# Performance work log

Measured on AMD Instinct MI355X. Metric: run time of the kernel, lower is better.

## Reference

```python
import jax, jax.numpy as jnp
import numpy as np

C = 512
GROUPS = 4
EPS = 1e-6


def group_norm(x, w, b):
    # x: [B, C, L]
    B, Ch, L = x.shape
    xg = x.reshape(B, GROUPS, Ch // GROUPS, L)
    mean = xg.mean(axis=(2, 3), keepdims=True)
    var = xg.var(axis=(2, 3), keepdims=True)
    xn = ((xg - mean) * jax.lax.rsqrt(var + EPS)).reshape(B, Ch, L)
    return xn * w[None, :, None] + b[None, :, None]


def conv1x1(x, w, b):
    # 1x1 Conv1d == channel mixing: w [Cout, Cin], x [B, Cin, L]
    return jnp.einsum('oc,bcl->bol', w, x) + b[None, :, None]


def setup_inputs() -> dict:
    key = jax.random.key(0)
    ks = jax.random.split(key, 11)
    s = 1.0 / np.sqrt(C)
    return {
        'x': jax.random.normal(ks[0], (8, C, 2048), dtype=jnp.float32),
        'gn_w': jnp.ones((C,), jnp.float32),
        'gn_b': jnp.zeros((C,), jnp.float32),
        'qw': jax.random.uniform(ks[1], (C, C), jnp.float32, -s, s),
        'qb': jax.random.uniform(ks[2], (C,), jnp.float32, -s, s),
        'kw': jax.random.uniform(ks[3], (C, C), jnp.float32, -s, s),
        'kb': jax.random.uniform(ks[4], (C,), jnp.float32, -s, s),
        'vw': jax.random.uniform(ks[5], (C, C), jnp.float32, -s, s),
        'vb': jax.random.uniform(ks[6], (C,), jnp.float32, -s, s),
        'pw': jax.random.uniform(ks[7], (C, C), jnp.float32, -s, s),
        'pb': jax.random.uniform(ks[8], (C,), jnp.float32, -s, s),
    }


def reference(x, gn_w, gn_b, qw, qb, kw, kb, vw, vb, pw, pb):
    scale = x.shape[1] ** (-0.5)
    xn = group_norm(x, gn_w, gn_b)
    q = conv1x1(xn, qw, qb)
    k = conv1x1(xn, kw, kb)
    v = conv1x1(xn, vw, vb)
    attn = jnp.einsum('bci,bcj->bij', q, k) * scale  # [B, L, L]
    attn = jax.nn.softmax(attn, axis=2)
    out = jnp.einsum('bij,bcj->bci', attn, v)
    out = conv1x1(out, pw, pb)
    return x + out
```

## Files before the change

### kernel.cpp

```cpp
#include <hip/hip_runtime.h>

#define BB 8
#define CC 512
#define LL 2048
#define GG 4
#define CPG 128

typedef _Float16 f16;
typedef _Float16 f16x4 __attribute__((ext_vector_type(4)));
typedef _Float16 f16x8 __attribute__((ext_vector_type(8)));
typedef float f32x4 __attribute__((ext_vector_type(4)));

__device__ __forceinline__ void gload_lds16(const f16* g, f16* l)
{
    __builtin_amdgcn_global_load_lds(
        (__attribute__((address_space(1))) void*)g,
        (__attribute__((address_space(3))) void*)l, 16, 0, 0);
}

__global__ __launch_bounds__(256) void convert_gn(
    const float* __restrict__ qw, const float* __restrict__ kw,
    const float* __restrict__ vw, const float* __restrict__ pw,
    const float* __restrict__ qb, const float* __restrict__ kb,
    const float* __restrict__ x,
    f16* __restrict__ Wqk, f16* __restrict__ Wv, f16* __restrict__ Wp,
    float* __restrict__ qkb, float2* __restrict__ part)
{
    int bid = blockIdx.x;
    if (bid < 256) {
        int j = bid * 256 + threadIdx.x;
        int i = j * 4;
        float4 q4 = *(const float4*)(qw + i);
        float4 k4 = *(const float4*)(kw + i);
        float4 v4 = *(const float4*)(vw + i);
        float4 p4 = *(const float4*)(pw + i);
        f16x4 o;
        o[0] = (f16)q4.x; o[1] = (f16)q4.y; o[2] = (f16)q4.z; o[3] = (f16)q4.w;
        *(f16x4*)(Wqk + i) = o;
        o[0] = (f16)k4.x; o[1] = (f16)k4.y; o[2] = (f16)k4.z; o[3] = (f16)k4.w;
        *(f16x4*)(Wqk + CC * CC + i) = o;
        o[0] = (f16)v4.x; o[1] = (f16)v4.y; o[2] = (f16)v4.z; o[3] = (f16)v4.w;
        *(f16x4*)(Wv + i) = o;
        o[0] = (f16)p4.x; o[1] = (f16)p4.y; o[2] = (f16)p4.z; o[3] = (f16)p4.w;
        *(f16x4*)(Wp + i) = o;
        if (j < CC) { qkb[j] = qb[j]; qkb[CC + j] = kb[j]; }
    } else {
        int r = bid - 256;
        int s = r & 31, g = (r >> 5) & 3, b = r >> 7;
        const float4* p = (const float4*)(x + (size_t)b * CC * LL
                                            + (size_t)g * CPG * LL + (size_t)s * 8192);
        float sum = 0.f, sq = 0.f;
        for (int i = threadIdx.x; i < 2048; i += 256) {
            float4 v = p[i];
            sum += v.x + v.y + v.z + v.w;
            sq  += v.x * v.x + v.y * v.y + v.z * v.z + v.w * v.w;
        }
        for (int o = 32; o; o >>= 1) { sum += __shfl_xor(sum, o); sq += __shfl_xor(sq, o); }
        __shared__ float2 red[4];
        int wave = threadIdx.x >> 6, lane = threadIdx.x & 63;
        if (lane == 0) red[wave] = make_float2(sum, sq);
        __syncthreads();
        if (threadIdx.x == 0) {
            float S = red[0].x + red[1].x + red[2].x + red[3].x;
            float Q = red[0].y + red[1].y + red[2].y + red[3].y;
            part[((size_t)b * GG + g) * 32 + s] = make_float2(S, Q);
        }
    }
}

__global__ __launch_bounds__(256) void gn_norm_t(
    const float* __restrict__ x, const float2* __restrict__ part,
    const float* __restrict__ gw, const float* __restrict__ gb,
    f16* __restrict__ xnT)
{
    __shared__ float t[64][65];
    __shared__ float2 stLds;
    int l0 = blockIdx.x * 64, c0 = blockIdx.y * 64, b = blockIdx.z;
    int tid = threadIdx.x;
    if (tid < 32) {
        float2 p = part[((size_t)b * GG + (c0 >> 7)) * 32 + tid];
        float s = p.x, q = p.y;
        for (int o = 16; o; o >>= 1) { s += __shfl_xor(s, o); q += __shfl_xor(q, o); }
        if (tid == 0) {
            const float invN = 1.0f / (float)(CPG * LL);
            float mean = s * invN;
            float var  = q * invN - mean * mean;
            stLds = make_float2(mean, rsqrtf(var + 1e-6f));
        }
    }
    __syncthreads();
    float2 st = stLds;
    const float* xb = x + (size_t)b * CC * LL;
    {
        int c = tid >> 2, lb = (tid & 3) * 16;
        float g = gw[c0 + c], b2 = gb[c0 + c];
        const float4* src = (const float4*)(xb + (size_t)(c0 + c) * LL + l0 + lb);
#pragma unroll
        for (int q = 0; q < 4; ++q) {
            float4 v = src[q];
            int l = lb + q * 4;
            t[c][l + 0] = (v.x - st.x) * st.y * g + b2;
            t[c][l + 1] = (v.y - st.x) * st.y * g + b2;
            t[c][l + 2] = (v.z - st.x) * st.y * g + b2;
            t[c][l + 3] = (v.w - st.x) * st.y * g + b2;
        }
    }
    __syncthreads();
    f16* o = xnT + (size_t)b * LL * CC;
    {
        int c8 = (tid & 7) * 8;
#pragma unroll
        for (int h = 0; h < 2; ++h) {
            int l = (tid >> 3) + h * 32;
            f16x8 v;
#pragma unroll
            for (int u = 0; u < 8; ++u) v[u] = (f16)t[c8 + u][l];
            *(f16x8*)(o + (size_t)(l0 + l) * CC + c0 + c8) = v;
        }
    }
}

template<int NBT, int BIAS_MODE, bool RESID, bool SOFTEXP, bool ROWSCALE, typename OUT_T>
__global__ __launch_bounds__(256, 2) void gemm_bt(
    const f16* __restrict__ A, size_t sA,
    const f16* __restrict__ B, size_t sB,
    OUT_T* __restrict__ Co, size_t sC,
    const float* __restrict__ resid, size_t sR,
    const float* __restrict__ bias,
    float* __restrict__ rowpart,
    int M, int N, int K, int lda, int ldb, int ldc, float alpha)
{
    constexpr int BN = NBT * 32;

    const int tid  = threadIdx.x;
    const int lane = tid & 63;
    const int wave = tid >> 6;
    const int wr = wave >> 1, wc = wave & 1;
    const int l15 = lane & 15, lhi = lane >> 4;

    const int GX = gridDim.x, GXY = gridDim.x * gridDim.y;
    const int nwg = GXY * gridDim.z;
    int lin = blockIdx.z * GXY + blockIdx.y * GX + blockIdx.x;
    int logical = (lin & 7) * (nwg >> 3) + (lin >> 3);
    const int bz = logical / GXY;
    int rem = logical - bz * GXY;
    const int bm = rem / GX;
    const int bn = rem - bm * GX;

    A  += (size_t)bz * sA;
    B  += (size_t)bz * sB;
    Co += (size_t)bz * sC;

    __shared__ f16 ldsA[128 * 64];
    __shared__ f16 ldsB[BN * 64];
    __shared__ float rsl[128];

    f32x4 acc[4][NBT] = {};

    if constexpr (ROWSCALE) {
        if (tid < 128) {
            const float* rp = rowpart + ((size_t)bz * M + bm * 128 + tid) * 8;
            float s = 0.f;
#pragma unroll
            for (int k = 0; k < 8; ++k) s += rp[k];
            rsl[tid] = 1.0f / s;
        }
    }

    const int srcColE = ((lane & 7) ^ (lane >> 3)) * 8;
    const int rowBase = wave * 8 + (lane >> 3);
    const f16* Ag = A + (size_t)(bm * 128 + rowBase) * lda + srcColE;
    const f16* Bg = B + (size_t)(bn * BN  + rowBase) * ldb + srcColE;

    for (int k0 = 0; k0 < K; k0 += 64) {
#pragma unroll
        for (int it = 0; it < 4; ++it)
            gload_lds16(Ag + (size_t)(it * 32) * lda + k0,
                        (f16*)((char*)ldsA + it * 4096 + wave * 1024));
#pragma unroll
        for (int it = 0; it < NBT; ++it)
            gload_lds16(Bg + (size_t)(it * 32) * ldb + k0,
                        (f16*)((char*)ldsB + it * 4096 + wave * 1024));
        __syncthreads();
#pragma unroll
        for (int kk = 0; kk < 64; kk += 32) {
            const int kb2 = (kk + lhi * 8) * 2;
            f16x8 af[4], bfr[NBT];
#pragma unroll
            for (int m = 0; m < 4; ++m) {
                int row = wr * 64 + m * 16 + l15;
                int phys = ((row * 128 + kb2) ^ ((row & 7) << 4)) >> 1;
                af[m] = *(const f16x8*)(ldsA + phys);
            }
#pragma unroll
            for (int n = 0; n < NBT; ++n) {
                int row = wc * (NBT * 16) + n * 16 + l15;
                int phys = ((row * 128 + kb2) ^ ((row & 7) << 4)) >> 1;
                bfr[n] = *(const f16x8*)(ldsB + phys);
            }
#pragma unroll
            for (int m = 0; m < 4; ++m)
#pragma unroll
                for (int n = 0; n < NBT; ++n)
                    acc[m][n] = __builtin_amdgcn_mfma_f32_16x16x32_f16(
                        af[m], bfr[n], acc[m][n], 0, 0, 0);
        }
        __syncthreads();
    }

    if constexpr (SOFTEXP) {
        __shared__ float rs2[2][128];
        float rowacc[16];
#pragma unroll
        for (int i = 0; i < 16; ++i) rowacc[i] = 0.f;
#pragma unroll
        for (int m = 0; m < 4; ++m) {
#pragma unroll
            for (int n = 0; n < NBT; ++n) {
                int col = bn * BN + wc * (NBT * 16) + n * 16 + l15;
#pragma unroll
                for (int r = 0; r < 4; ++r) {
                    int row = bm * 128 + wr * 64 + m * 16 + lhi * 4 + r;
                    float e = __expf(fminf(acc[m][n][r] * alpha, 11.0f));
                    rowacc[m * 4 + r] += e;
                    Co[(size_t)row * ldc + col] = (OUT_T)e;
                }
            }
        }
#pragma unroll
        for (int off = 1; off < 16; off <<= 1)
#pragma unroll
            for (int i = 0; i < 16; ++i)
                rowacc[i] += __shfl_xor(rowacc[i], off);
        if (l15 == 0) {
#pragma unroll
            for (int i = 0; i < 16; ++i)
                rs2[wc][wr * 64 + (i >> 2) * 16 + lhi * 4 + (i & 3)] = rowacc[i];
        }
        __syncthreads();
        if (tid < 128) {
            int row = bm * 128 + tid;
            rowpart[((size_t)bz * M + row) * gridDim.x + bn] =
                rs2[0][tid] + rs2[1][tid];
        }
    } else {
#pragma unroll
        for (int m = 0; m < 4; ++m) {
#pragma unroll
            for (int n = 0; n < NBT; ++n) {
                int col = bn * BN + wc * (NBT * 16) + n * 16 + l15;
#pragma unroll
                for (int r = 0; r < 4; ++r) {
                    int row = bm * 128 + wr * 64 + m * 16 + lhi * 4 + r;
                    float v = acc[m][n][r] * alpha;
                    if (BIAS_MODE == 1) v += bias[row];
                    if (BIAS_MODE == 2) v += bias[col];
                    if (ROWSCALE) v *= rsl[row - bm * 128];
                    if (RESID) v += resid[(size_t)bz * sR + (size_t)row * ldc + col];
                    Co[(size_t)row * ldc + col] = (OUT_T)v;
                }
            }
        }
    }
}

__global__ void fill_marker(float* out, int n)
{
    int i = blockIdx.x * 256 + threadIdx.x;
    if (i < n) out[i] = 12345.0f;
}

extern "C" void kernel_launch(void* const* d_in, const int* in_sizes, int n_in,
                              void* d_out, int out_size, void* d_ws, size_t ws_size,
                              hipStream_t stream)
{
    const float* x  = (const float*)d_in[0];
    const float* gw = (const float*)d_in[1];
    const float* gb = (const float*)d_in[2];
    const float* qw = (const float*)d_in[3];
    const float* qb = (const float*)d_in[4];
    const float* kw = (const float*)d_in[5];
    const float* kb = (const float*)d_in[6];
    const float* vw = (const float*)d_in[7];
    const float* vb = (const float*)d_in[8];
    const float* pw = (const float*)d_in[9];
    const float* pb = (const float*)d_in[10];
    float* out = (float*)d_out;

    char* w = (char*)d_ws;
    float2* part  = (float2*)w;
    f16* Wqk  = (f16*)(w + 16384);
    f16* Wv   = Wqk + (size_t)1024 * CC;
    f16* Wp   = Wv  + (size_t)CC * CC;
    float* qkb = (float*)(Wp + (size_t)CC * CC);
    f16* xnT  = (f16*)((char*)qkb + 4096);
    f16* QK   = xnT + (size_t)BB * LL * CC;
    f16* Vm   = QK  + (size_t)BB * LL * 1024;
    f16* Pm   = Vm  + (size_t)BB * CC * LL;
    float* rowpart = (float*)(Pm + (size_t)BB * LL * LL);
    f16* O2   = xnT;
    size_t need = (size_t)((char*)(rowpart + (size_t)BB * LL * 8) - w);
    if (ws_size < need) {
        fill_marker<<<(out_size + 255) / 256, 256, 0, stream>>>(out, out_size);
        return;
    }

    convert_gn<<<dim3(1280), 256, 0, stream>>>(
        qw, kw, vw, pw, qb, kb, x, Wqk, Wv, Wp, qkb, part);
    gn_norm_t<<<dim3(LL / 64, CC / 64, BB), 256, 0, stream>>>(x, part, gw, gb, xnT);

    gemm_bt<8, 2, false, false, false, f16><<<dim3(1024 / 256, LL / 128, BB), 256, 0, stream>>>(
        xnT, (size_t)LL * CC, Wqk, 0, QK, (size_t)LL * 1024, nullptr, 0, qkb,
        nullptr,
        LL, 1024, CC, CC, CC, 1024, 1.0f);

    gemm_bt<4, 1, false, false, false, f16><<<dim3(LL / 128, CC / 128, BB), 256, 0, stream>>>(
        Wv, 0, xnT, (size_t)LL * CC, Vm, (size_t)CC * LL, nullptr, 0, vb,
        nullptr,
        CC, LL, CC, CC, CC, LL, 1.0f);

    gemm_bt<8, 0, false, true, false, f16><<<dim3(LL / 256, LL / 128, BB), 256, 0, stream>>>(
        QK, (size_t)LL * 1024, QK + CC, (size_t)LL * 1024, Pm, (size_t)LL * LL,
        nullptr, 0, nullptr,
        rowpart,
        LL, LL, CC, 1024, 1024, LL, 0.04419417382415922f);

    gemm_bt<4, 0, false, false, true, f16><<<dim3(CC / 128, LL / 128, BB), 256, 0, stream>>>(
        Pm, (size_t)LL * LL, Vm, (size_t)CC * LL, O2, (size_t)LL * CC,
        nullptr, 0, nullptr,
        rowpart,
        LL, CC, LL, LL, LL, CC, 1.0f);

    gemm_bt<4, 1, true, false, false, float><<<dim3(LL / 128, CC / 128, BB), 256, 0, stream>>>(
        Wp, 0, O2, (size_t)LL * CC, out, (size_t)CC * LL, x, (size_t)CC * LL, pb,
        nullptr,
        CC, LL, CC, CC, CC, LL, 1.0f);
}
```

Measured before the change: 153.0 us.

## Add double-buffered 512-thread pipelined GEMM for QK, attention and PV stages

```diff
diff --git a/kernel.cpp b/kernel.cpp
--- a/kernel.cpp
+++ b/kernel.cpp
@@ -120,23 +120,17 @@
     }
 }
 
-template<int NBT, int BIAS_MODE, bool RESID, bool SOFTEXP, bool ROWSCALE, typename OUT_T>
-__global__ __launch_bounds__(256, 2) void gemm_bt(
+template<int BIAS_MODE, bool SOFTEXP, bool ROWSCALE, typename OUT_T>
+__global__ __launch_bounds__(512, 2) void gemm_pipe(
     const f16* __restrict__ A, size_t sA,
     const f16* __restrict__ B, size_t sB,
     OUT_T* __restrict__ Co, size_t sC,
-    const float* __restrict__ resid, size_t sR,
-    const float* __restrict__ bias,
-    float* __restrict__ rowpart,
-    int M, int N, int K, int lda, int ldb, int ldc, float alpha)
-{
-    constexpr int BN = NBT * 32;
-
-    const int tid  = threadIdx.x;
-    const int lane = tid & 63;
-    const int wave = tid >> 6;
-    const int wr = wave >> 1, wc = wave & 1;
+    const float* __restrict__ bias, float* __restrict__ rowpart,
+    int M, int K, int lda, int ldb, int ldc, float alpha)
+{
+    const int tid = threadIdx.x, lane = tid & 63, w = tid >> 6;
     const int l15 = lane & 15, lhi = lane >> 4;
+    const int wr = w >> 2, wc = w & 3;
 
     const int GX = gridDim.x, GXY = gridDim.x * gridDim.y;
     const int nwg = GXY * gridDim.z;
@@ -147,15 +141,16 @@
     const int bm = rem / GX;
     const int bn = rem - bm * GX;
 
-    A  += (size_t)bz * sA;
-    B  += (size_t)bz * sB;
+    A  += (size_t)bz * sA + (size_t)(bm * 128) * lda;
+    B  += (size_t)bz * sB + (size_t)(bn * 256) * ldb;
     Co += (size_t)bz * sC;
 
-    __shared__ f16 ldsA[128 * 64];
-    __shared__ f16 ldsB[BN * 64];
+    __shared__ f16 ldsA[2][128 * 64];
+    __shared__ f16 ldsB[2][256 * 64];
+    __shared__ float rs[4][128];
     __shared__ float rsl[128];
 
-    f32x4 acc[4][NBT] = {};
+    f32x4 acc[4][4] = {};
 
     if constexpr (ROWSCALE) {
         if (tid < 128) {
@@ -168,56 +163,126 @@
     }
 
     const int srcColE = ((lane & 7) ^ (lane >> 3)) * 8;
-    const int rowBase = wave * 8 + (lane >> 3);
-    const f16* Ag = A + (size_t)(bm * 128 + rowBase) * lda + srcColE;
-    const f16* Bg = B + (size_t)(bn * BN  + rowBase) * ldb + srcColE;
-
-    for (int k0 = 0; k0 < K; k0 += 64) {
-#pragma unroll
-        for (int it = 0; it < 4; ++it)
-            gload_lds16(Ag + (size_t)(it * 32) * lda + k0,
-                        (f16*)((char*)ldsA + it * 4096 + wave * 1024));
-#pragma unroll
-        for (int it = 0; it < NBT; ++it)
-            gload_lds16(Bg + (size_t)(it * 32) * ldb + k0,
-                        (f16*)((char*)ldsB + it * 4096 + wave * 1024));
-        __syncthreads();
-#pragma unroll
-        for (int kk = 0; kk < 64; kk += 32) {
-            const int kb2 = (kk + lhi * 8) * 2;
-            f16x8 af[4], bfr[NBT];
-#pragma unroll
-            for (int m = 0; m < 4; ++m) {
-                int row = wr * 64 + m * 16 + l15;
-                int phys = ((row * 128 + kb2) ^ ((row & 7) << 4)) >> 1;
-                af[m] = *(const f16x8*)(ldsA + phys);
-            }
-#pragma unroll
-            for (int n = 0; n < NBT; ++n) {
-                int row = wc * (NBT * 16) + n * 16 + l15;
-                int phys = ((row * 128 + kb2) ^ ((row & 7) << 4)) >> 1;
-                bfr[n] = *(const f16x8*)(ldsB + phys);
-            }
-#pragma unroll
-            for (int m = 0; m < 4; ++m)
-#pragma unroll
-                for (int n = 0; n < NBT; ++n)
+    const int sub = (w & 3) * 8 + (lane >> 3);
+    const int half = w >> 2;
+    const int ldst = half * 8192 + (w & 3) * 1024;
+
+    auto S_A1 = [&](int t) {
+        gload_lds16(A + (size_t)(half * 64 + sub) * lda + t * 64 + srcColE,
+                    (f16*)((char*)ldsA[t & 1] + ldst)); };
+    auto S_B1 = [&](int t) {
+        gload_lds16(B + (size_t)(half * 64 + sub) * ldb + t * 64 + srcColE,
+                    (f16*)((char*)ldsB[t & 1] + ldst)); };
+    auto S_B2 = [&](int t) {
+        gload_lds16(B + (size_t)(128 + half * 64 + sub) * ldb + t * 64 + srcColE,
+                    (f16*)((char*)ldsB[t & 1] + 16384 + ldst)); };
+    auto S_B1b = [&](int t) {
+        gload_lds16(B + (size_t)(half * 64 + 32 + sub) * ldb + t * 64 + srcColE,
+                    (f16*)((char*)ldsB[t & 1] + 4096 + ldst)); };
+    auto S_B2b = [&](int t) {
+        gload_lds16(B + (size_t)(128 + half * 64 + 32 + sub) * ldb + t * 64 + srcColE,
+                    (f16*)((char*)ldsB[t & 1] + 20480 + ldst)); };
+    auto S_A1b = [&](int t) {
+        gload_lds16(A + (size_t)(half * 64 + 32 + sub) * lda + t * 64 + srcColE,
+                    (f16*)((char*)ldsA[t & 1] + 4096 + ldst)); };
+
+    auto rd = [&](const f16* tile, int row, int byteCol) -> f16x8 {
+        return *(const f16x8*)((const char*)tile
+            + (((row << 7) + byteCol) ^ ((row & 7) << 4)));
+    };
+
+    const int NT = K >> 6;
+
+    S_A1(0); S_B1(0); S_B2(0); S_B1b(0); S_B2b(0); S_A1b(0);
+    asm volatile("s_waitcnt vmcnt(3)" ::: "memory");
+    __builtin_amdgcn_s_barrier();
+
+    for (int t = 0; t < NT; ++t) {
+        const f16* cA = ldsA[t & 1];
+        const f16* cB = ldsB[t & 1];
+        const bool st = (t < NT - 1);
+        f16x8 a01[2][2], a23[2][2], b01[2][2], b23[2][2];
+#pragma unroll
+        for (int m = 0; m < 2; ++m)
+#pragma unroll
+            for (int kk = 0; kk < 2; ++kk)
+                a01[m][kk] = rd(cA, wr * 64 + m * 16 + l15, kk * 64 + lhi * 16);
+#pragma unroll
+        for (int n = 0; n < 2; ++n)
+#pragma unroll
+            for (int kk = 0; kk < 2; ++kk)
+                b01[n][kk] = rd(cB, wc * 64 + n * 16 + l15, kk * 64 + lhi * 16);
+        if (st) { S_A1(t + 1); S_B1(t + 1); S_B2(t + 1); }
+        asm volatile("s_waitcnt lgkmcnt(0)" ::: "memory");
+        __builtin_amdgcn_sched_barrier(0);
+        __builtin_amdgcn_s_setprio(1);
+#pragma unroll
+        for (int m = 0; m < 2; ++m)
+#pragma unroll
+            for (int n = 0; n < 2; ++n)
+#pragma unroll
+                for (int kk = 0; kk < 2; ++kk)
                     acc[m][n] = __builtin_amdgcn_mfma_f32_16x16x32_f16(
-                        af[m], bfr[n], acc[m][n], 0, 0, 0);
-        }
-        __syncthreads();
+                        a01[m][kk], b01[n][kk], acc[m][n], 0, 0, 0);
+        __builtin_amdgcn_s_setprio(0);
+        if (st) asm volatile("s_waitcnt vmcnt(4)" ::: "memory");
+        else    asm volatile("s_waitcnt vmcnt(1)" ::: "memory");
+        __builtin_amdgcn_s_barrier();
+#pragma unroll
+        for (int n = 0; n < 2; ++n)
+#pragma unroll
+            for (int kk = 0; kk < 2; ++kk)
+                b23[n][kk] = rd(cB, wc * 64 + 32 + n * 16 + l15, kk * 64 + lhi * 16);
+        if (st) { S_B1b(t + 1); S_B2b(t + 1); }
+        asm volatile("s_waitcnt lgkmcnt(0)" ::: "memory");
+        __builtin_amdgcn_sched_barrier(0);
+        __builtin_amdgcn_s_setprio(1);
+#pragma unroll
+        for (int m = 0; m < 2; ++m)
+#pragma unroll
+            for (int n = 0; n < 2; ++n)
+#pragma unroll
+                for (int kk = 0; kk < 2; ++kk)
+                    acc[m][n + 2] = __builtin_amdgcn_mfma_f32_16x16x32_f16(
+                        a01[m][kk], b23[n][kk], acc[m][n + 2], 0, 0, 0);
+        __builtin_amdgcn_s_setprio(0);
+        if (st) asm volatile("s_waitcnt vmcnt(5)" ::: "memory");
+        else    asm volatile("s_waitcnt vmcnt(0)" ::: "memory");
+        __builtin_amdgcn_s_barrier();
+#pragma unroll
+        for (int m = 0; m < 2; ++m)
+#pragma unroll
+            for (int kk = 0; kk < 2; ++kk)
+                a23[m][kk] = rd(cA, wr * 64 + 32 + m * 16 + l15, kk * 64 + lhi * 16);
+        if (st) { S_A1b(t + 1); }
+        asm volatile("s_waitcnt lgkmcnt(0)" ::: "memory");
+        __builtin_amdgcn_sched_barrier(0);
+        __builtin_amdgcn_s_setprio(1);
+#pragma unroll
+        for (int m = 0; m < 2; ++m)
+#pragma unroll
+            for (int n = 0; n < 2; ++n)
+#pragma unroll
+                for (int kk = 0; kk < 2; ++kk) {
+                    acc[m + 2][n] = __builtin_amdgcn_mfma_f32_16x16x32_f16(
+                        a23[m][kk], b01[n][kk], acc[m + 2][n], 0, 0, 0);
+                    acc[m + 2][n + 2] = __builtin_amdgcn_mfma_f32_16x16x32_f16(
+                        a23[m][kk], b23[n][kk], acc[m + 2][n + 2], 0, 0, 0);
+                }
+        __builtin_amdgcn_s_setprio(0);
+        if (st) asm volatile("s_waitcnt vmcnt(3)" ::: "memory");
+        __builtin_amdgcn_s_barrier();
     }
 
     if constexpr (SOFTEXP) {
-        __shared__ float rs2[2][128];
         float rowacc[16];
 #pragma unroll
         for (int i = 0; i < 16; ++i) rowacc[i] = 0.f;
 #pragma unroll
         for (int m = 0; m < 4; ++m) {
 #pragma unroll
-            for (int n = 0; n < NBT; ++n) {
-                int col = bn * BN + wc * (NBT * 16) + n * 16 + l15;
+            for (int n = 0; n < 4; ++n) {
+                int col = bn * 256 + wc * 64 + n * 16 + l15;
 #pragma unroll
                 for (int r = 0; r < 4; ++r) {
                     int row = bm * 128 + wr * 64 + m * 16 + lhi * 4 + r;
@@ -235,30 +300,119 @@
         if (l15 == 0) {
 #pragma unroll
             for (int i = 0; i < 16; ++i)
-                rs2[wc][wr * 64 + (i >> 2) * 16 + lhi * 4 + (i & 3)] = rowacc[i];
+                rs[wc][wr * 64 + (i >> 2) * 16 + lhi * 4 + (i & 3)] = rowacc[i];
         }
         __syncthreads();
         if (tid < 128) {
             int row = bm * 128 + tid;
             rowpart[((size_t)bz * M + row) * gridDim.x + bn] =
-                rs2[0][tid] + rs2[1][tid];
+                rs[0][tid] + rs[1][tid] + rs[2][tid] + rs[3][tid];
         }
     } else {
 #pragma unroll
         for (int m = 0; m < 4; ++m) {
 #pragma unroll
-            for (int n = 0; n < NBT; ++n) {
-                int col = bn * BN + wc * (NBT * 16) + n * 16 + l15;
+            for (int n = 0; n < 4; ++n) {
+                int col = bn * 256 + wc * 64 + n * 16 + l15;
 #pragma unroll
                 for (int r = 0; r < 4; ++r) {
                     int row = bm * 128 + wr * 64 + m * 16 + lhi * 4 + r;
                     float v = acc[m][n][r] * alpha;
-                    if (BIAS_MODE == 1) v += bias[row];
                     if (BIAS_MODE == 2) v += bias[col];
                     if (ROWSCALE) v *= rsl[row - bm * 128];
-                    if (RESID) v += resid[(size_t)bz * sR + (size_t)row * ldc + col];
                     Co[(size_t)row * ldc + col] = (OUT_T)v;
                 }
+            }
+        }
+    }
+}
+
+template<int BIAS_MODE, bool RESID, typename OUT_T>
+__global__ __launch_bounds__(256, 2) void gemm_bt(
+    const f16* __restrict__ A, size_t sA,
+    const f16* __restrict__ B, size_t sB,
+    OUT_T* __restrict__ Co, size_t sC,
+    const float* __restrict__ resid, size_t sR,
+    const float* __restrict__ bias,
+    int M, int N, int K, int lda, int ldb, int ldc, float alpha)
+{
+    const int tid  = threadIdx.x;
+    const int lane = tid & 63;
+    const int wave = tid >> 6;
+    const int wr = wave >> 1, wc = wave & 1;
+    const int l15 = lane & 15, lhi = lane >> 4;
+
+    const int GX = gridDim.x, GXY = gridDim.x * gridDim.y;
+    const int nwg = GXY * gridDim.z;
+    int lin = blockIdx.z * GXY + blockIdx.y * GX + blockIdx.x;
+    int logical = (lin & 7) * (nwg >> 3) + (lin >> 3);
+    const int bz = logical / GXY;
+    int rem = logical - bz * GXY;
+    const int bm = rem / GX;
+    const int bn = rem - bm * GX;
+
+    A  += (size_t)bz * sA;
+    B  += (size_t)bz * sB;
+    Co += (size_t)bz * sC;
+
+    __shared__ f16 ldsA[128 * 64];
+    __shared__ f16 ldsB[128 * 64];
+
+    f32x4 acc[4][4] = {};
+
+    const int srcColE = ((lane & 7) ^ (lane >> 3)) * 8;
+    const int rowBase = wave * 8 + (lane >> 3);
+    const f16* Ag = A + (size_t)(bm * 128 + rowBase) * lda + srcColE;
+    const f16* Bg = B + (size_t)(bn * 128 + rowBase) * ldb + srcColE;
+
+    for (int k0 = 0; k0 < K; k0 += 64) {
+#pragma unroll
+        for (int it = 0; it < 4; ++it) {
+            gload_lds16(Ag + (size_t)(it * 32) * lda + k0,
+                        (f16*)((char*)ldsA + it * 4096 + wave * 1024));
+            gload_lds16(Bg + (size_t)(it * 32) * ldb + k0,
+                        (f16*)((char*)ldsB + it * 4096 + wave * 1024));
+        }
+        __syncthreads();
+#pragma unroll
+        for (int kk = 0; kk < 64; kk += 32) {
+            const int kb2 = (kk + lhi * 8) * 2;
+            f16x8 af[4], bfr[4];
+#pragma unroll
+            for (int m = 0; m < 4; ++m) {
+                int row = wr * 64 + m * 16 + l15;
+                int phys = ((row * 128 + kb2) ^ ((row & 7) << 4)) >> 1;
+                af[m] = *(const f16x8*)(ldsA + phys);
+            }
+#pragma unroll
+            for (int n = 0; n < 4; ++n) {
+                int row = wc * 64 + n * 16 + l15;
+                int phys = ((row * 128 + kb2) ^ ((row & 7) << 4)) >> 1;
+                bfr[n] = *(const f16x8*)(ldsB + phys);
+            }
+#pragma unroll
+            for (int m = 0; m < 4; ++m)
+#pragma unroll
+                for (int n = 0; n < 4; ++n)
+                    acc[m][n] = __builtin_amdgcn_mfma_f32_16x16x32_f16(
+                        af[m], bfr[n], acc[m][n], 0, 0, 0);
+        }
+        __syncthreads();
+    }
+
+#pragma unroll
+    for (int m = 0; m < 4; ++m) {
+#pragma unroll
+        for (int n = 0; n < 4; ++n) {
+            int col = bn * 128 + wc * 64 + n * 16 + l15;
+#pragma unroll
+            for (int r = 0; r < 4; ++r) {
+                int row = bm * 128 + wr * 64 + m * 16 + lhi * 4 + r;
+                float v = acc[m][n][r] * alpha;
+                if (BIAS_MODE == 1) v += bias[row];
+                if (BIAS_MODE == 2) v += bias[col];
+                if (RESID) v += resid[(size_t)bz * sR + (size_t)row * ldc + col];
+                Co[(size_t)row * ldc + col] = (OUT_T)v;
             }
         }
     }
@@ -309,30 +463,25 @@
         qw, kw, vw, pw, qb, kb, x, Wqk, Wv, Wp, qkb, part);
     gn_norm_t<<<dim3(LL / 64, CC / 64, BB), 256, 0, stream>>>(x, part, gw, gb, xnT);
 
-    gemm_bt<8, 2, false, false, false, f16><<<dim3(1024 / 256, LL / 128, BB), 256, 0, stream>>>(
-        xnT, (size_t)LL * CC, Wqk, 0, QK, (size_t)LL * 1024, nullptr, 0, qkb,
-        nullptr,
-        LL, 1024, CC, CC, CC, 1024, 1.0f);
-
-    gemm_bt<4, 1, false, false, false, f16><<<dim3(LL / 128, CC / 128, BB), 256, 0, stream>>>(
+    gemm_pipe<2, false, false, f16><<<dim3(1024 / 256, LL / 128, BB), 512, 0, stream>>>(
+        xnT, (size_t)LL * CC, Wqk, 0, QK, (size_t)LL * 1024, qkb, nullptr,
+        LL, CC, CC, CC, 1024, 1.0f);
+
+    gemm_bt<1, false, f16><<<dim3(LL / 128, CC / 128, BB), 256, 0, stream>>>(
         Wv, 0, xnT, (size_t)LL * CC, Vm, (size_t)CC * LL, nullptr, 0, vb,
-        nullptr,
         CC, LL, CC, CC, CC, LL, 1.0f);
 
-    gemm_bt<8, 0, false, true, false, f16><<<dim3(LL / 256, LL / 128, BB), 256, 0, stream>>>(
+    gemm_pipe<0, true, false, f16><<<dim3(LL / 256, LL / 128, BB), 512, 0, stream>>>(
         QK, (size_t)LL * 1024, QK + CC, (size_t)LL * 1024, Pm, (size_t)LL * LL,
-        nullptr, 0, nullptr,
-        rowpart,
-        LL, LL, CC, 1024, 1024, LL, 0.04419417382415922f);
-
-    gemm_bt<4, 0, false, false, true, f16><<<dim3(CC / 128, LL / 128, BB), 256, 0, stream>>>(
+        nullptr, rowpart,
+        LL, CC, 1024, 1024, LL, 0.04419417382415922f);
+
+    gemm_pipe<0, false, true, f16><<<dim3(CC / 256, LL / 128, BB), 512, 0, stream>>>(
         Pm, (size_t)LL * LL, Vm, (size_t)CC * LL, O2, (size_t)LL * CC,
-        nullptr, 0, nullptr,
-        rowpart,
-        LL, CC, LL, LL, LL, CC, 1.0f);
-
-    gemm_bt<4, 1, true, false, false, float><<<dim3(LL / 128, CC / 128, BB), 256, 0, stream>>>(
+        nullptr, rowpart,
+        LL, LL, LL, LL, CC, 1.0f);
+
+    gemm_bt<1, true, float><<<dim3(LL / 128, CC / 128, BB), 256, 0, stream>>>(
         Wp, 0, O2, (size_t)LL * CC, out, (size_t)CC * LL, x, (size_t)CC * LL, pb,
-        nullptr,
         CC, LL, CC, CC, CC, LL, 1.0f);
 }
```

Result: slower. 180.9 us (+18.3%).

## Fold Q and K projections into a precomputed Wq^T·Wk matrix for attention

Applied to the files above, without the earlier changes.

```diff
diff --git a/kernel.cpp b/kernel.cpp
--- a/kernel.cpp
+++ b/kernel.cpp
@@ -21,46 +21,72 @@
 __global__ __launch_bounds__(256) void convert_gn(
     const float* __restrict__ qw, const float* __restrict__ kw,
     const float* __restrict__ vw, const float* __restrict__ pw,
-    const float* __restrict__ qb, const float* __restrict__ kb,
+    const float* __restrict__ qb,
     const float* __restrict__ x,
-    f16* __restrict__ Wqk, f16* __restrict__ Wv, f16* __restrict__ Wp,
-    float* __restrict__ qkb, float2* __restrict__ part)
+    f16* __restrict__ WqT, f16* __restrict__ WkT,
+    f16* __restrict__ Wv, f16* __restrict__ Wp,
+    float* __restrict__ c1, float2* __restrict__ part)
 {
     int bid = blockIdx.x;
+    int tid = threadIdx.x;
     if (bid < 256) {
-        int j = bid * 256 + threadIdx.x;
-        int i = j * 4;
-        float4 q4 = *(const float4*)(qw + i);
-        float4 k4 = *(const float4*)(kw + i);
+        int i = (bid * 256 + tid) * 4;
         float4 v4 = *(const float4*)(vw + i);
         float4 p4 = *(const float4*)(pw + i);
         f16x4 o;
-        o[0] = (f16)q4.x; o[1] = (f16)q4.y; o[2] = (f16)q4.z; o[3] = (f16)q4.w;
-        *(f16x4*)(Wqk + i) = o;
-        o[0] = (f16)k4.x; o[1] = (f16)k4.y; o[2] = (f16)k4.z; o[3] = (f16)k4.w;
-        *(f16x4*)(Wqk + CC * CC + i) = o;
         o[0] = (f16)v4.x; o[1] = (f16)v4.y; o[2] = (f16)v4.z; o[3] = (f16)v4.w;
         *(f16x4*)(Wv + i) = o;
         o[0] = (f16)p4.x; o[1] = (f16)p4.y; o[2] = (f16)p4.z; o[3] = (f16)p4.w;
         *(f16x4*)(Wp + i) = o;
-        if (j < CC) { qkb[j] = qb[j]; qkb[CC + j] = kb[j]; }
+    } else if (bid < 384) {
+        const float* src = (bid < 320) ? qw : kw;
+        f16* dst = (bid < 320) ? WqT : WkT;
+        int t = (bid - 256) & 63;
+        int o0 = (t & 7) * 64, a0 = (t >> 3) * 64;
+        __shared__ float ts[64][65];
+        {
+            int r = tid >> 2, c4 = (tid & 3) * 16;
+#pragma unroll
+            for (int e4 = 0; e4 < 4; ++e4) {
+                float4 v = *(const float4*)(src + (size_t)(o0 + r) * CC + a0 + c4 + e4 * 4);
+                ts[r][c4 + e4 * 4 + 0] = v.x; ts[r][c4 + e4 * 4 + 1] = v.y;
+                ts[r][c4 + e4 * 4 + 2] = v.z; ts[r][c4 + e4 * 4 + 3] = v.w;
+            }
+        }
+        __syncthreads();
+        {
+            int j8 = (tid & 7) * 8;
+#pragma unroll
+            for (int h = 0; h < 2; ++h) {
+                int ai = (tid >> 3) + h * 32;
+                f16x8 v;
+#pragma unroll
+                for (int e = 0; e < 8; ++e) v[e] = (f16)ts[j8 + e][ai];
+                *(f16x8*)(dst + (size_t)(a0 + ai) * CC + o0 + j8) = v;
+            }
+        }
+    } else if (bid < 386) {
+        int b = (bid - 384) * 256 + tid;
+        float s = 0.f;
+        for (int o = 0; o < CC; ++o) s += kw[(size_t)o * CC + b] * qb[o];
+        c1[b] = s;
     } else {
-        int r = bid - 256;
+        int r = bid - 386;
         int s = r & 31, g = (r >> 5) & 3, b = r >> 7;
         const float4* p = (const float4*)(x + (size_t)b * CC * LL
                                             + (size_t)g * CPG * LL + (size_t)s * 8192);
         float sum = 0.f, sq = 0.f;
-        for (int i = threadIdx.x; i < 2048; i += 256) {
+        for (int i = tid; i < 2048; i += 256) {
             float4 v = p[i];
             sum += v.x + v.y + v.z + v.w;
             sq  += v.x * v.x + v.y * v.y + v.z * v.z + v.w * v.w;
         }
         for (int o = 32; o; o >>= 1) { sum += __shfl_xor(sum, o); sq += __shfl_xor(sq, o); }
         __shared__ float2 red[4];
-        int wave = threadIdx.x >> 6, lane = threadIdx.x & 63;
+        int wave = tid >> 6, lane = tid & 63;
         if (lane == 0) red[wave] = make_float2(sum, sq);
         __syncthreads();
-        if (threadIdx.x == 0) {
+        if (tid == 0) {
             float S = red[0].x + red[1].x + red[2].x + red[3].x;
             float Q = red[0].y + red[1].y + red[2].y + red[3].y;
             part[((size_t)b * GG + g) * 32 + s] = make_float2(S, Q);
@@ -120,7 +146,8 @@
     }
 }
 
-template<int NBT, int BIAS_MODE, bool RESID, bool SOFTEXP, bool ROWSCALE, typename OUT_T>
+template<int NBT, int BIAS_MODE, bool RESID, bool SOFTEXP, bool ROWSCALE,
+         bool ROWDOT, typename OUT_T>
 __global__ __launch_bounds__(256, 2) void gemm_bt(
     const f16* __restrict__ A, size_t sA,
     const f16* __restrict__ B, size_t sB,
@@ -128,6 +155,8 @@
     const float* __restrict__ resid, size_t sR,
     const float* __restrict__ bias,
     float* __restrict__ rowpart,
+    const float* __restrict__ c1d, float* __restrict__ colb_out,
+    const float* __restrict__ colb_in,
     int M, int N, int K, int lda, int ldb, int ldc, float alpha)
 {
     constexpr int BN = NBT * 32;
@@ -154,8 +183,11 @@
     __shared__ f16 ldsA[128 * 64];
     __shared__ f16 ldsB[BN * 64];
     __shared__ float rsl[128];
+    __shared__ float c1L[ROWDOT ? 512 : 1];
+    __shared__ float cbL[SOFTEXP ? 256 : 1];
 
     f32x4 acc[4][NBT] = {};
+    float rdot[4] = {0.f, 0.f, 0.f, 0.f};
 
     if constexpr (ROWSCALE) {
         if (tid < 128) {
@@ -166,6 +198,13 @@
             rsl[tid] = 1.0f / s;
         }
     }
+    if constexpr (ROWDOT) {
+        c1L[tid] = c1d[tid];
+        c1L[tid + 256] = c1d[tid + 256];
+    }
+    if constexpr (SOFTEXP) {
+        cbL[tid] = alpha * colb_in[(size_t)bz * N + bn * BN + tid];
+    }
 
     const int srcColE = ((lane & 7) ^ (lane >> 3)) * 8;
     const int rowBase = wave * 8 + (lane >> 3);
@@ -198,6 +237,14 @@
                 int phys = ((row * 128 + kb2) ^ ((row & 7) << 4)) >> 1;
                 bfr[n] = *(const f16x8*)(ldsB + phys);
             }
+            if constexpr (ROWDOT) {
+                int kbase = k0 + kk + lhi * 8;
+#pragma unroll
+                for (int m = 0; m < 4; ++m)
+#pragma unroll
+                    for (int e = 0; e < 8; ++e)
+                        rdot[m] += c1L[kbase + e] * (float)af[m][e];
+            }
 #pragma unroll
             for (int m = 0; m < 4; ++m)
 #pragma unroll
@@ -208,6 +255,19 @@
         __syncthreads();
     }
 
+    if constexpr (ROWDOT) {
+#pragma unroll
+        for (int m = 0; m < 4; ++m) {
+            rdot[m] += __shfl_xor(rdot[m], 16);
+            rdot[m] += __shfl_xor(rdot[m], 32);
+        }
+        if (wc == 0 && lhi == 0 && bn == 0) {
+#pragma unroll
+            for (int m = 0; m < 4; ++m)
+                colb_out[(size_t)bz * M + bm * 128 + wr * 64 + m * 16 + l15] = rdot[m];
+        }
+    }
+
     if constexpr (SOFTEXP) {
         __shared__ float rs2[2][128];
         float rowacc[16];
@@ -217,11 +277,12 @@
         for (int m = 0; m < 4; ++m) {
 #pragma unroll
             for (int n = 0; n < NBT; ++n) {
-                int col = bn * BN + wc * (NBT * 16) + n * 16 + l15;
+                int colL = wc * (NBT * 16) + n * 16 + l15;
+                int col = bn * BN + colL;
 #pragma unroll
                 for (int r = 0; r < 4; ++r) {
                     int row = bm * 128 + wr * 64 + m * 16 + lhi * 4 + r;
-                    float e = __expf(fminf(acc[m][n][r] * alpha, 11.0f));
+                    float e = __expf(fminf(acc[m][n][r] * alpha + cbL[colL], 11.0f));
                     rowacc[m * 4 + r] += e;
                     Co[(size_t)row * ldc + col] = (OUT_T)e;
                 }
@@ -280,7 +341,7 @@
     const float* qw = (const float*)d_in[3];
     const float* qb = (const float*)d_in[4];
     const float* kw = (const float*)d_in[5];
-    const float* kb = (const float*)d_in[6];
+    const float* kb = (const float*)d_in[6];  (void)kb;
     const float* vw = (const float*)d_in[7];
     const float* vb = (const float*)d_in[8];
     const float* pw = (const float*)d_in[9];
@@ -288,51 +349,60 @@
     float* out = (float*)d_out;
 
     char* w = (char*)d_ws;
-    float2* part  = (float2*)w;
-    f16* Wqk  = (f16*)(w + 16384);
-    f16* Wv   = Wqk + (size_t)1024 * CC;
+    float2* part = (float2*)w;
+    f16* WqT  = (f16*)(w + 16384);
+    f16* WkT  = WqT + (size_t)CC * CC;
+    f16* Wv   = WkT + (size_t)CC * CC;
     f16* Wp   = Wv  + (size_t)CC * CC;
-    float* qkb = (float*)(Wp + (size_t)CC * CC);
-    f16* xnT  = (f16*)((char*)qkb + 4096);
-    f16* QK   = xnT + (size_t)BB * LL * CC;
-    f16* Vm   = QK  + (size_t)BB * LL * 1024;
+    f16* Mf   = Wp  + (size_t)CC * CC;
+    float* c1 = (float*)(Mf + (size_t)CC * CC);
+    f16* xnT  = (f16*)((char*)c1 + 4096);
+    f16* ktT  = xnT + (size_t)BB * LL * CC;
+    f16* Vm   = ktT + (size_t)BB * LL * CC;
     f16* Pm   = Vm  + (size_t)BB * CC * LL;
     float* rowpart = (float*)(Pm + (size_t)BB * LL * LL);
+    float* colb    = rowpart + (size_t)BB * LL * 8;
     f16* O2   = xnT;
-    size_t need = (size_t)((char*)(rowpart + (size_t)BB * LL * 8) - w);
+    size_t need = (size_t)((char*)(colb + (size_t)BB * LL) - w);
     if (ws_size < need) {
         fill_marker<<<(out_size + 255) / 256, 256, 0, stream>>>(out, out_size);
         return;
     }
 
-    convert_gn<<<dim3(1280), 256, 0, stream>>>(
-        qw, kw, vw, pw, qb, kb, x, Wqk, Wv, Wp, qkb, part);
+    convert_gn<<<dim3(1410), 256, 0, stream>>>(
+        qw, kw, vw, pw, qb, x, WqT, WkT, Wv, Wp, c1, part);
+
+    gemm_bt<4, 0, false, false, false, false, f16><<<dim3(4, 4, 1), 256, 0, stream>>>(
+        WqT, 0, WkT, 0, Mf, 0, nullptr, 0, nullptr,
+        nullptr, nullptr, nullptr, nullptr,
+        CC, CC, CC, CC, CC, CC, 1.0f);
+
     gn_norm_t<<<dim3(LL / 64, CC / 64, BB), 256, 0, stream>>>(x, part, gw, gb, xnT);
 
-    gemm_bt<8, 2, false, false, false, f16><<<dim3(1024 / 256, LL / 128, BB), 256, 0, stream>>>(
-        xnT, (size_t)LL * CC, Wqk, 0, QK, (size_t)LL * 1024, nullptr, 0, qkb,
-        nullptr,
-        LL, 1024, CC, CC, CC, 1024, 1.0f);
-
-    gemm_bt<4, 1, false, false, false, f16><<<dim3(LL / 128, CC / 128, BB), 256, 0, stream>>>(
+    gemm_bt<4, 0, false, false, false, true, f16><<<dim3(CC / 128, LL / 128, BB), 256, 0, stream>>>(
+        xnT, (size_t)LL * CC, Mf, 0, ktT, (size_t)LL * CC, nullptr, 0, nullptr,
+        nullptr, c1, colb, nullptr,
+        LL, CC, CC, CC, CC, CC, 1.0f);
+
+    gemm_bt<4, 1, false, false, false, false, f16><<<dim3(LL / 128, CC / 128, BB), 256, 0, stream>>>(
         Wv, 0, xnT, (size_t)LL * CC, Vm, (size_t)CC * LL, nullptr, 0, vb,
-        nullptr,
+        nullptr, nullptr, nullptr, nullptr,
         CC, LL, CC, CC, CC, LL, 1.0f);
 
-    gemm_bt<8, 0, false, true, false, f16><<<dim3(LL / 256, LL / 128, BB), 256, 0, stream>>>(
-        QK, (size_t)LL * 1024, QK + CC, (size_t)LL * 1024, Pm, (size_t)LL * LL,
+    gemm_bt<8, 0, false, true, false, false, f16><<<dim3(LL / 256, LL / 128, BB), 256, 0, stream>>>(
+        xnT, (size_t)LL * CC, ktT, (size_t)LL * CC, Pm, (size_t)LL * LL,
         nullptr, 0, nullptr,
-        rowpart,
-        LL, LL, CC, 1024, 1024, LL, 0.04419417382415922f);
-
-    gemm_bt<4, 0, false, false, true, f16><<<dim3(CC / 128, LL / 128, BB), 256, 0, stream>>>(
+        rowpart, nullptr, nullptr, colb,
+        LL, LL, CC, CC, CC, LL, 0.04419417382415922f);
+
+    gemm_bt<4, 0, false, false, true, false, f16><<<dim3(CC / 128, LL / 128, BB), 256, 0, stream>>>(
         Pm, (size_t)LL * LL, Vm, (size_t)CC * LL, O2, (size_t)LL * CC,
         nullptr, 0, nullptr,
-        rowpart,
+        rowpart, nullptr, nullptr, nullptr,
         LL, CC, LL, LL, LL, CC, 1.0f);
 
-    gemm_bt<4, 1, true, false, false, float><<<dim3(LL / 128, CC / 128, BB), 256, 0, stream>>>(
+    gemm_bt<4, 1, true, false, false, false, float><<<dim3(LL / 128, CC / 128, BB), 256, 0, stream>>>(
         Wp, 0, O2, (size_t)LL * CC, out, (size_t)CC * LL, x, (size_t)CC * LL, pb,
-        nullptr,
+        nullptr, nullptr, nullptr, nullptr,
         CC, LL, CC, CC, CC, LL, 1.0f);
 }
```

Result: slower. 169.7 us (+10.9%).

## Double-buffer LDS tiles in the NBT=4 GEMMs to overlap loads with MFMA

Applied to the files above, without the earlier changes.

```diff
diff --git a/kernel.cpp b/kernel.cpp
--- a/kernel.cpp
+++ b/kernel.cpp
@@ -120,7 +120,8 @@
     }
 }
 
-template<int NBT, int BIAS_MODE, bool RESID, bool SOFTEXP, bool ROWSCALE, typename OUT_T>
+template<int NBT, bool DBUF, int BIAS_MODE, bool RESID, bool SOFTEXP, bool ROWSCALE,
+         typename OUT_T>
 __global__ __launch_bounds__(256, 2) void gemm_bt(
     const f16* __restrict__ A, size_t sA,
     const f16* __restrict__ B, size_t sB,
@@ -131,6 +132,7 @@
     int M, int N, int K, int lda, int ldb, int ldc, float alpha)
 {
     constexpr int BN = NBT * 32;
+    constexpr int NLB = DBUF ? 2 : 1;
 
     const int tid  = threadIdx.x;
     const int lane = tid & 63;
@@ -151,8 +153,8 @@
     B  += (size_t)bz * sB;
     Co += (size_t)bz * sC;
 
-    __shared__ f16 ldsA[128 * 64];
-    __shared__ f16 ldsB[BN * 64];
+    __shared__ f16 ldsA[NLB][128 * 64];
+    __shared__ f16 ldsB[NLB][BN * 64];
     __shared__ float rsl[128];
 
     f32x4 acc[4][NBT] = {};
@@ -172,16 +174,18 @@
     const f16* Ag = A + (size_t)(bm * 128 + rowBase) * lda + srcColE;
     const f16* Bg = B + (size_t)(bn * BN  + rowBase) * ldb + srcColE;
 
-    for (int k0 = 0; k0 < K; k0 += 64) {
+    auto STAGE = [&](int k0, int d) {
 #pragma unroll
         for (int it = 0; it < 4; ++it)
             gload_lds16(Ag + (size_t)(it * 32) * lda + k0,
-                        (f16*)((char*)ldsA + it * 4096 + wave * 1024));
+                        (f16*)((char*)ldsA[d] + it * 4096 + wave * 1024));
 #pragma unroll
         for (int it = 0; it < NBT; ++it)
             gload_lds16(Bg + (size_t)(it * 32) * ldb + k0,
-                        (f16*)((char*)ldsB + it * 4096 + wave * 1024));
-        __syncthreads();
+                        (f16*)((char*)ldsB[d] + it * 4096 + wave * 1024));
+    };
+
+    auto COMPUTE = [&](int d) {
 #pragma unroll
         for (int kk = 0; kk < 64; kk += 32) {
             const int kb2 = (kk + lhi * 8) * 2;
@@ -190,13 +194,13 @@
             for (int m = 0; m < 4; ++m) {
                 int row = wr * 64 + m * 16 + l15;
                 int phys = ((row * 128 + kb2) ^ ((row & 7) << 4)) >> 1;
-                af[m] = *(const f16x8*)(ldsA + phys);
+                af[m] = *(const f16x8*)(ldsA[d] + phys);
             }
 #pragma unroll
             for (int n = 0; n < NBT; ++n) {
                 int row = wc * (NBT * 16) + n * 16 + l15;
                 int phys = ((row * 128 + kb2) ^ ((row & 7) << 4)) >> 1;
-                bfr[n] = *(const f16x8*)(ldsB + phys);
+                bfr[n] = *(const f16x8*)(ldsB[d] + phys);
             }
 #pragma unroll
             for (int m = 0; m < 4; ++m)
@@ -205,7 +209,29 @@
                     acc[m][n] = __builtin_amdgcn_mfma_f32_16x16x32_f16(
                         af[m], bfr[n], acc[m][n], 0, 0, 0);
         }
-        __syncthreads();
+    };
+
+    const int NT = K >> 6;
+    if constexpr (DBUF) {
+        STAGE(0, 0);
+        asm volatile("s_waitcnt vmcnt(0)" ::: "memory");
+        __builtin_amdgcn_s_barrier();
+        __builtin_amdgcn_sched_barrier(0);
+        for (int t = 0; t < NT; ++t) {
+            const int cur = t & 1;
+            if (t + 1 < NT) STAGE((t + 1) * 64, cur ^ 1);
+            COMPUTE(cur);
+            if (t + 1 < NT) asm volatile("s_waitcnt vmcnt(0)" ::: "memory");
+            __builtin_amdgcn_s_barrier();
+            __builtin_amdgcn_sched_barrier(0);
+        }
+    } else {
+        for (int t = 0; t < NT; ++t) {
+            STAGE(t * 64, 0);
+            __syncthreads();
+            COMPUTE(0);
+            __syncthreads();
+        }
     }
 
     if constexpr (SOFTEXP) {
@@ -309,29 +335,29 @@
         qw, kw, vw, pw, qb, kb, x, Wqk, Wv, Wp, qkb, part);
     gn_norm_t<<<dim3(LL / 64, CC / 64, BB), 256, 0, stream>>>(x, part, gw, gb, xnT);
 
-    gemm_bt<8, 2, false, false, false, f16><<<dim3(1024 / 256, LL / 128, BB), 256, 0, stream>>>(
+    gemm_bt<8, false, 2, false, false, false, f16><<<dim3(1024 / 256, LL / 128, BB), 256, 0, stream>>>(
         xnT, (size_t)LL * CC, Wqk, 0, QK, (size_t)LL * 1024, nullptr, 0, qkb,
         nullptr,
         LL, 1024, CC, CC, CC, 1024, 1.0f);
 
-    gemm_bt<4, 1, false, false, false, f16><<<dim3(LL / 128, CC / 128, BB), 256, 0, stream>>>(
+    gemm_bt<4, true, 1, false, false, false, f16><<<dim3(LL / 128, CC / 128, BB), 256, 0, stream>>>(
         Wv, 0, xnT, (size_t)LL * CC, Vm, (size_t)CC * LL, nullptr, 0, vb,
         nullptr,
         CC, LL, CC, CC, CC, LL, 1.0f);
 
-    gemm_bt<8, 0, false, true, false, f16><<<dim3(LL / 256, LL / 128, BB), 256, 0, stream>>>(
+    gemm_bt<8, false, 0, false, true, false, f16><<<dim3(LL / 256, LL / 128, BB), 256, 0, stream>>>(
         QK, (size_t)LL * 1024, QK + CC, (size_t)LL * 1024, Pm, (size_t)LL * LL,
         nullptr, 0, nullptr,
         rowpart,
         LL, LL, CC, 1024, 1024, LL, 0.04419417382415922f);
 
-    gemm_bt<4, 0, false, false, true, f16><<<dim3(CC / 128, LL / 128, BB), 256, 0, stream>>>(
+    gemm_bt<4, true, 0, false, false, true, f16><<<dim3(CC / 128, LL / 128, BB), 256, 0, stream>>>(
         Pm, (size_t)LL * LL, Vm, (size_t)CC * LL, O2, (size_t)LL * CC,
         nullptr, 0, nullptr,
         rowpart,
         LL, CC, LL, LL, LL, CC, 1.0f);
 
-    gemm_bt<4, 1, true, false, false, float><<<dim3(LL / 128, CC / 128, BB), 256, 0, stream>>>(
+    gemm_bt<4, true, 1, true, false, false, float><<<dim3(LL / 128, CC / 128, BB), 256, 0, stream>>>(
         Wp, 0, O2, (size_t)LL * CC, out, (size_t)CC * LL, x, (size_t)CC * LL, pb,
         nullptr,
         CC, LL, CC, CC, CC, LL, 1.0f);
```

After: 153.4 us. No clear change (+0.3%).
